# Optimization experiments

Hardware: AMD Instinct MI355X
Metric: run time of the kernel (lower is better)

The kernel has to match this reference:

```python
import jax, jax.numpy as jnp
import numpy as np

B, N, P, F = 4, 131072, 512, 32  # batch, points per batch, plane_size, feature_dim


def setup_inputs() -> dict:
    key = jax.random.key(0)
    k1, k2 = jax.random.split(key)
    coords = jax.random.uniform(k1, (B, N, 3), jnp.float32, -1.0, 1.0)
    # torch.nn.init.uniform_(tplanes, -0.01, 0.01)
    tplanes = jax.random.uniform(k2, (3, P, P, F), jnp.float32, -0.01, 0.01)
    return {"coords": coords, "tplanes": tplanes}


def _bilerp(plane, uv):
    # plane: [P, P, F] laid out [H(v), W(u), C]; uv: [M, 2] in [0, 1]
    # matches nvdiffrast texture(filter_mode='linear', boundary_mode='clamp',
    # max_mip_level=0): texel centers at (i + 0.5) / P, clamp-to-edge.
    Ps = plane.shape[0]
    x = jnp.clip(uv[:, 0] * Ps - 0.5, 0.0, Ps - 1.0)
    y = jnp.clip(uv[:, 1] * Ps - 0.5, 0.0, Ps - 1.0)
    x0f = jnp.floor(x)
    y0f = jnp.floor(y)
    xi0 = x0f.astype(jnp.int32)
    yi0 = y0f.astype(jnp.int32)
    xi1 = jnp.minimum(xi0 + 1, Ps - 1)
    yi1 = jnp.minimum(yi0 + 1, Ps - 1)
    fx = (x - x0f)[:, None]  # [M, 1]
    fy = (y - y0f)[:, None]
    f00 = plane[yi0, xi0]  # [M, F]
    f01 = plane[yi0, xi1]
    f10 = plane[yi1, xi0]
    f11 = plane[yi1, xi1]
    return (f00 * (1.0 - fx) + f01 * fx) * (1.0 - fy) + (f10 * (1.0 - fx) + f11 * fx) * fy


def reference(coords, tplanes):
    batch_size = coords.shape[0]
    c = coords * 0.5 + 0.5          # [-1,1] -> [0,1]
    c = c.reshape(-1, 3)            # [M, 3]
    # plane 0 samples (x, y); plane 1 samples (x, z); plane 2 samples (z, y)
    uvs = jnp.stack([c[:, (0, 1)], c[:, (0, 2)], c[:, (2, 1)]], axis=0)  # [3, M, 2]
    feats = jax.vmap(_bilerp)(tplanes, uvs)        # [3, M, F]
    feats = jnp.transpose(feats, (1, 0, 2))        # [M, 3, F]
    out = feats.reshape(batch_size, -1, 3 * F)     # concat over planes: [B, N, 3F]
    return out
```

## Files before the change

kernel.cpp:

```cpp
#include <hip/hip_runtime.h>


#define PS 512
#define FDIM 32

typedef float    floatx4 __attribute__((ext_vector_type(4)));
typedef _Float16 halfx8  __attribute__((ext_vector_type(8)));

__global__ __launch_bounds__(256) void convert_kernel(
    const floatx4* __restrict__ in,
    halfx8* __restrict__ out8,
    int n8)
{
    int t = blockIdx.x * blockDim.x + threadIdx.x;
    if (t >= n8) return;
    floatx4 a = in[2 * t];
    floatx4 b = in[2 * t + 1];
    halfx8 h;
    h[0] = (_Float16)a.x; h[1] = (_Float16)a.y;
    h[2] = (_Float16)a.z; h[3] = (_Float16)a.w;
    h[4] = (_Float16)b.x; h[5] = (_Float16)b.y;
    h[6] = (_Float16)b.z; h[7] = (_Float16)b.w;
    out8[t] = h;
}

__global__ __launch_bounds__(256) void tplanes_enc_fp16_kernel(
    const float* __restrict__ coords,
    const _Float16* __restrict__ tp16,
    float* __restrict__ out,
    int total)
{
    int tid = blockIdx.x * blockDim.x + threadIdx.x;
    if (tid >= total) return;

    int chunk = tid & 3;
    int pp    = tid >> 2;
    int plane = pp % 3;
    int point = pp / 3;

    float cx = coords[point * 3 + 0] * 0.5f + 0.5f;
    float cy = coords[point * 3 + 1] * 0.5f + 0.5f;
    float cz = coords[point * 3 + 2] * 0.5f + 0.5f;

    float u = (plane == 2) ? cz : cx;
    float v = (plane == 1) ? cz : cy;

    float x = fminf(fmaxf(u * (float)PS - 0.5f, 0.0f), (float)(PS - 1));
    float y = fminf(fmaxf(v * (float)PS - 0.5f, 0.0f), (float)(PS - 1));
    float x0f = floorf(x);
    float y0f = floorf(y);
    int xi0 = (int)x0f;
    int yi0 = (int)y0f;
    int xi1 = min(xi0 + 1, PS - 1);
    int yi1 = min(yi0 + 1, PS - 1);
    float fx = x - x0f;
    float fy = y - y0f;

    const halfx8* base = (const halfx8*)tp16 + (size_t)plane * PS * PS * (FDIM / 8);
    int o00 = (yi0 * PS + xi0) * 4 + chunk;
    int o01 = (yi0 * PS + xi1) * 4 + chunk;
    int o10 = (yi1 * PS + xi0) * 4 + chunk;
    int o11 = (yi1 * PS + xi1) * 4 + chunk;

    halfx8 f00 = base[o00];
    halfx8 f01 = base[o01];
    halfx8 f10 = base[o10];
    halfx8 f11 = base[o11];

    float gx = 1.0f - fx;
    float gy = 1.0f - fy;

    floatx4 r0, r1;
#pragma unroll
    for (int j = 0; j < 4; ++j) {
        r0[j] = ((float)f00[j] * gx + (float)f01[j] * fx) * gy
              + ((float)f10[j] * gx + (float)f11[j] * fx) * fy;
    }
#pragma unroll
    for (int j = 0; j < 4; ++j) {
        r1[j] = ((float)f00[j + 4] * gx + (float)f01[j + 4] * fx) * gy
              + ((float)f10[j + 4] * gx + (float)f11[j + 4] * fx) * fy;
    }

    int ob = pp * 8 + chunk * 2;
    __builtin_nontemporal_store(r0, (floatx4*)out + ob);
    __builtin_nontemporal_store(r1, (floatx4*)out + ob + 1);
}

__global__ __launch_bounds__(256) void tplanes_enc_f32_kernel(
    const float* __restrict__ coords,
    const float* __restrict__ tplanes,
    float* __restrict__ out,
    int total)
{
    int tid = blockIdx.x * blockDim.x + threadIdx.x;
    if (tid >= total) return;

    int chunk = tid & 7;
    int pp    = tid >> 3;
    int plane = pp % 3;
    int point = pp / 3;

    float cx = coords[point * 3 + 0] * 0.5f + 0.5f;
    float cy = coords[point * 3 + 1] * 0.5f + 0.5f;
    float cz = coords[point * 3 + 2] * 0.5f + 0.5f;
    float u = (plane == 2) ? cz : cx;
    float v = (plane == 1) ? cz : cy;

    float x = fminf(fmaxf(u * (float)PS - 0.5f, 0.0f), (float)(PS - 1));
    float y = fminf(fmaxf(v * (float)PS - 0.5f, 0.0f), (float)(PS - 1));
    float x0f = floorf(x);
    float y0f = floorf(y);
    int xi0 = (int)x0f;
    int yi0 = (int)y0f;
    int xi1 = min(xi0 + 1, PS - 1);
    int yi1 = min(yi0 + 1, PS - 1);
    float fx = x - x0f;
    float fy = y - y0f;

    const floatx4* base = (const floatx4*)(tplanes + (size_t)plane * PS * PS * FDIM);
    int o00 = (yi0 * PS + xi0) * 8 + chunk;
    int o01 = (yi0 * PS + xi1) * 8 + chunk;
    int o10 = (yi1 * PS + xi0) * 8 + chunk;
    int o11 = (yi1 * PS + xi1) * 8 + chunk;

    floatx4 f00 = base[o00];
    floatx4 f01 = base[o01];
    floatx4 f10 = base[o10];
    floatx4 f11 = base[o11];

    float gx = 1.0f - fx;
    float gy = 1.0f - fy;
    floatx4 r;
    r.x = (f00.x * gx + f01.x * fx) * gy + (f10.x * gx + f11.x * fx) * fy;
    r.y = (f00.y * gx + f01.y * fx) * gy + (f10.y * gx + f11.y * fx) * fy;
    r.z = (f00.z * gx + f01.z * fx) * gy + (f10.z * gx + f11.z * fx) * fy;
    r.w = (f00.w * gx + f01.w * fx) * gy + (f10.w * gx + f11.w * fx) * fy;
    __builtin_nontemporal_store(r, (floatx4*)out + (size_t)pp * 8 + chunk);
}

extern "C" void kernel_launch(void* const* d_in, const int* in_sizes, int n_in,
                              void* d_out, int out_size, void* d_ws, size_t ws_size,
                              hipStream_t stream) {
    const float* coords  = (const float*)d_in[0];
    const float* tplanes = (const float*)d_in[1];
    float* out = (float*)d_out;

    int M = in_sizes[0] / 3;
    const size_t planesN = (size_t)3 * PS * PS * FDIM;
    const size_t need    = planesN * sizeof(_Float16);

    int block = 256;
    if (ws_size >= need) {
        int n8 = (int)(planesN / 8);
        int g1 = (n8 + block - 1) / block;
        convert_kernel<<<g1, block, 0, stream>>>(
            (const floatx4*)tplanes, (halfx8*)d_ws, n8);

        int total = M * 3 * 4;
        int g2 = (total + block - 1) / block;
        tplanes_enc_fp16_kernel<<<g2, block, 0, stream>>>(
            coords, (const _Float16*)d_ws, out, total);
    } else {
        int total = M * 3 * 8;
        int g = (total + block - 1) / block;
        tplanes_enc_f32_kernel<<<g, block, 0, stream>>>(coords, tplanes, out, total);
    }
}
```

Baseline: 361.8 us.

## Pack horizontally adjacent texel pairs into contiguous fp16 records for sampling

The conversion kernel now writes, for every texel, a 128-byte record holding its own fp16 features followed by those of its right neighbour (clamped at the edge). The sampling kernel then fetches the two horizontal taps of each row from one contiguous record, so its four gathers touch two memory regions instead of up to four. In exchange the workspace doubles in size and the conversion pass writes twice as much data.

Result: faster. 336.8 us (-6.9%).

```diff
diff --git a/kernel.cpp b/kernel.cpp
--- a/kernel.cpp
+++ b/kernel.cpp
@@ -7,26 +7,34 @@
 typedef float    floatx4 __attribute__((ext_vector_type(4)));
 typedef _Float16 halfx8  __attribute__((ext_vector_type(8)));
 
-__global__ __launch_bounds__(256) void convert_kernel(
+__global__ __launch_bounds__(256) void convert_pairs_kernel(
     const floatx4* __restrict__ in,
     halfx8* __restrict__ out8,
-    int n8)
+    int nthreads)
 {
     int t = blockIdx.x * blockDim.x + threadIdx.x;
-    if (t >= n8) return;
-    floatx4 a = in[2 * t];
-    floatx4 b = in[2 * t + 1];
+    if (t >= nthreads) return;
+    int sub  = t & 7;
+    int pair = t >> 3;
+    int x    = pair & (PS - 1);
+    int rowb = pair - x;
+    int tx   = min(x + (sub >> 2), PS - 1);
+    int c    = sub & 3;
+
+    size_t src = (size_t)(rowb + tx) * (FDIM / 4) + (size_t)c * 2;
+    floatx4 a = in[src];
+    floatx4 b = in[src + 1];
     halfx8 h;
     h[0] = (_Float16)a.x; h[1] = (_Float16)a.y;
     h[2] = (_Float16)a.z; h[3] = (_Float16)a.w;
     h[4] = (_Float16)b.x; h[5] = (_Float16)b.y;
     h[6] = (_Float16)b.z; h[7] = (_Float16)b.w;
-    out8[t] = h;
+    out8[(size_t)pair * 8 + sub] = h;
 }
 
-__global__ __launch_bounds__(256) void tplanes_enc_fp16_kernel(
+__global__ __launch_bounds__(256) void tplanes_enc_pair_kernel(
     const float* __restrict__ coords,
-    const _Float16* __restrict__ tp16,
+    const halfx8* __restrict__ pairs,
     float* __restrict__ out,
     int total)
 {
@@ -51,21 +59,17 @@
     float y0f = floorf(y);
     int xi0 = (int)x0f;
     int yi0 = (int)y0f;
-    int xi1 = min(xi0 + 1, PS - 1);
     int yi1 = min(yi0 + 1, PS - 1);
     float fx = x - x0f;
     float fy = y - y0f;
 
-    const halfx8* base = (const halfx8*)tp16 + (size_t)plane * PS * PS * (FDIM / 8);
-    int o00 = (yi0 * PS + xi0) * 4 + chunk;
-    int o01 = (yi0 * PS + xi1) * 4 + chunk;
-    int o10 = (yi1 * PS + xi0) * 4 + chunk;
-    int o11 = (yi1 * PS + xi1) * 4 + chunk;
+    size_t pair0 = (size_t)((plane * PS + yi0) * PS + xi0) * 8;
+    size_t pair1 = (size_t)((plane * PS + yi1) * PS + xi0) * 8;
 
-    halfx8 f00 = base[o00];
-    halfx8 f01 = base[o01];
-    halfx8 f10 = base[o10];
-    halfx8 f11 = base[o11];
+    halfx8 f00 = pairs[pair0 + chunk];
+    halfx8 f01 = pairs[pair0 + 4 + chunk];
+    halfx8 f10 = pairs[pair1 + chunk];
+    halfx8 f11 = pairs[pair1 + 4 + chunk];
 
     float gx = 1.0f - fx;
     float gy = 1.0f - fy;
@@ -147,20 +151,20 @@
     float* out = (float*)d_out;
 
     int M = in_sizes[0] / 3;
-    const size_t planesN = (size_t)3 * PS * PS * FDIM;
-    const size_t need    = planesN * sizeof(_Float16);
+    const size_t npairs = (size_t)3 * PS * PS;
+    const size_t need   = npairs * 128;
 
     int block = 256;
     if (ws_size >= need) {
-        int n8 = (int)(planesN / 8);
-        int g1 = (n8 + block - 1) / block;
-        convert_kernel<<<g1, block, 0, stream>>>(
-            (const floatx4*)tplanes, (halfx8*)d_ws, n8);
+        int n1 = (int)(npairs * 8);
+        int g1 = (n1 + block - 1) / block;
+        convert_pairs_kernel<<<g1, block, 0, stream>>>(
+            (const floatx4*)tplanes, (halfx8*)d_ws, n1);
 
         int total = M * 3 * 4;
         int g2 = (total + block - 1) / block;
-        tplanes_enc_fp16_kernel<<<g2, block, 0, stream>>>(
-            coords, (const _Float16*)d_ws, out, total);
+        tplanes_enc_pair_kernel<<<g2, block, 0, stream>>>(
+            coords, (const halfx8*)d_ws, out, total);
     } else {
         int total = M * 3 * 8;
         int g = (total + block - 1) / block;
```
